# Optimization experiments

Measured on AMD Instinct MI355X. Metric: run time of the kernel, lower is better.

The kernel has to match this reference:

```python
import jax, jax.numpy as jnp
import numpy as np

# snnTorch Leaky defaults: beta decay, unit threshold, subtract reset, ATan surrogate grad
BETA = 0.9
THRESH = 1.0
ALPHA = 2.0  # ATan surrogate sharpness


@jax.custom_vjp
def atan_spike(u):
    """Heaviside forward, ATan surrogate backward (snnTorch default spike_grad)."""
    return (u > 0).astype(u.dtype)


def _atan_fwd(u):
    return atan_spike(u), u


def _atan_bwd(u, g):
    # snnTorch ATan: dS/dU = (alpha/2) / (1 + (pi/2 * alpha * U)^2)
    return (g * (ALPHA / 2) / (1 + (jnp.pi / 2 * ALPHA * u) ** 2),)


atan_spike.defvjp(_atan_fwd, _atan_bwd)


def setup_inputs() -> dict:
    key = jax.random.key(0)
    # [T, B, C, H, W] input spike train (values in [0,1))
    x = jax.random.uniform(key, (16, 32, 64, 32, 32), dtype=jnp.float32)
    return {"x": x}


def reference(x):
    """LIF scan over the leading time dim T.

    mem_t = beta * mem_{t-1} + x_t - stop_grad(spk_{t-1}) * threshold  (subtract reset)
    spk_t = Heaviside(mem_t - threshold)  (ATan surrogate in backward)
    Returns spikes of shape [T, B, C, H, W].
    """
    zeros = jnp.zeros_like(x[0])

    def step(carry, x_t):
        mem, spk = carry
        mem = BETA * mem + x_t - jax.lax.stop_gradient(spk) * THRESH
        spk = atan_spike(mem - THRESH)
        return (mem, spk), spk

    _, spikes = jax.lax.scan(step, (zeros, zeros), x)
    return spikes
```

## Files before the change

kernel.cpp:

```cpp
#include <hip/hip_runtime.h>


constexpr int   T      = 16;
constexpr float BETA   = 0.9f;
constexpr float THRESH = 1.0f;

typedef float f4 __attribute__((ext_vector_type(4)));

__global__ __launch_bounds__(256) void lif_kernel(const float* __restrict__ x,
                                                  float* __restrict__ out,
                                                  int n_per_t) {
#pragma clang fp contract(off)
    const int idx = (blockIdx.x * blockDim.x + threadIdx.x) * 4;
    if (idx >= n_per_t) return;

    f4 v[T];

#pragma unroll
    for (int t = 0; t < T; ++t) {
        v[t] = *reinterpret_cast<const f4*>(x + (size_t)t * (size_t)n_per_t + (size_t)idx);
    }
    __builtin_amdgcn_sched_barrier(0);

    f4 mem = (f4)(0.f);
    f4 spk = (f4)(0.f);
#pragma unroll
    for (int t = 0; t < T; ++t) {
#pragma unroll
        for (int j = 0; j < 4; ++j) {
            mem[j] = BETA * mem[j] + v[t][j] - spk[j] * THRESH;
            spk[j] = (mem[j] - THRESH) > 0.f ? 1.f : 0.f;
        }
        __builtin_nontemporal_store(spk,
            reinterpret_cast<f4*>(out + (size_t)t * (size_t)n_per_t + (size_t)idx));
    }
}

extern "C" void kernel_launch(void* const* d_in, const int* in_sizes, int n_in,
                              void* d_out, int out_size, void* d_ws, size_t ws_size,
                              hipStream_t stream) {
    const float* x   = (const float*)d_in[0];
    float*       out = (float*)d_out;

    const int total   = in_sizes[0];
    const int n_per_t = total / T;
    const int threads = n_per_t / 4;

    dim3 block(256);
    dim3 grid((threads + block.x - 1) / block.x);
    lif_kernel<<<grid, block, 0, stream>>>(x, out, n_per_t);
}
```

Before: 251.1 us.

## Grid-stride LIF kernel with software-pipelined prefetch of next chunk

```diff
diff --git a/kernel.cpp b/kernel.cpp
--- a/kernel.cpp
+++ b/kernel.cpp
@@ -7,32 +7,49 @@
 
 typedef float f4 __attribute__((ext_vector_type(4)));
 
-__global__ __launch_bounds__(256) void lif_kernel(const float* __restrict__ x,
-                                                  float* __restrict__ out,
-                                                  int n_per_t) {
+__global__ __launch_bounds__(256, 4) void lif_kernel(const float* __restrict__ x,
+                                                     float* __restrict__ out,
+                                                     int n_per_t) {
 #pragma clang fp contract(off)
-    const int idx = (blockIdx.x * blockDim.x + threadIdx.x) * 4;
-    if (idx >= n_per_t) return;
+    const int tid      = blockIdx.x * blockDim.x + threadIdx.x;
+    const int nthreads = gridDim.x * blockDim.x;
+
+    const size_t np   = (size_t)n_per_t;
+    const size_t step = (size_t)nthreads * 4;
+    size_t       idx  = (size_t)tid * 4;
+    if (idx >= np) return;
 
     f4 v[T];
 
 #pragma unroll
     for (int t = 0; t < T; ++t) {
-        v[t] = *reinterpret_cast<const f4*>(x + (size_t)t * (size_t)n_per_t + (size_t)idx);
+        v[t] = *reinterpret_cast<const f4*>(x + (size_t)t * np + idx);
     }
-    __builtin_amdgcn_sched_barrier(0);
 
-    f4 mem = (f4)(0.f);
-    f4 spk = (f4)(0.f);
+#pragma clang loop unroll(disable)
+    for (;;) {
+        const size_t nidx = idx + step;
+        const bool   more = nidx < np;
+
+        f4 mem = (f4)(0.f);
+        f4 spk = (f4)(0.f);
 #pragma unroll
-    for (int t = 0; t < T; ++t) {
+        for (int t = 0; t < T; ++t) {
+            const f4 xt = v[t];
+            if (more) {
+                v[t] = *reinterpret_cast<const f4*>(x + (size_t)t * np + nidx);
+            }
 #pragma unroll
-        for (int j = 0; j < 4; ++j) {
-            mem[j] = BETA * mem[j] + v[t][j] - spk[j] * THRESH;
-            spk[j] = (mem[j] - THRESH) > 0.f ? 1.f : 0.f;
+            for (int j = 0; j < 4; ++j) {
+                mem[j] = BETA * mem[j] + xt[j] - spk[j] * THRESH;
+                spk[j] = (mem[j] - THRESH) > 0.f ? 1.f : 0.f;
+            }
+            __builtin_nontemporal_store(spk,
+                reinterpret_cast<f4*>(out + (size_t)t * np + idx));
         }
-        __builtin_nontemporal_store(spk,
-            reinterpret_cast<f4*>(out + (size_t)t * (size_t)n_per_t + (size_t)idx));
+
+        if (!more) break;
+        idx = nidx;
     }
 }
 
@@ -44,9 +61,10 @@
 
     const int total   = in_sizes[0];
     const int n_per_t = total / T;
-    const int threads = n_per_t / 4;
-
+    const int groups  = n_per_t / 4;
+    const int gpt     = 2;
+    const int threads = groups / gpt;
     dim3 block(256);
-    dim3 grid((threads + block.x - 1) / block.x);
+    dim3 grid(threads / block.x);
     lif_kernel<<<grid, block, 0, stream>>>(x, out, n_per_t);
 }
```

Result: no change. 246.7 us (-1.8%).
